# Kernel optimization log

Hardware: AMD Instinct MI355X
Metric: run time of the kernel (lower is better)

## Reference

```python
import jax, jax.numpy as jnp
import numpy as np
from jax import lax

B, T, N, H, M, L = 64, 12, 1000, 64, 4, 2


def _xavier(key, shape):
    fan_in, fan_out = shape[-2], shape[-1]
    scale = 1.414 * np.sqrt(2.0 / (fan_in + fan_out))
    return jax.random.normal(key, shape, dtype=jnp.float32) * scale


def setup_inputs() -> dict:
    key = jax.random.key(0)
    ks = jax.random.split(key, 20)
    inp = {
        "input": jax.random.normal(ks[0], (B, T, N, 1), dtype=jnp.float32),
        "init_hidden": jax.random.normal(ks[1], (L, B, N, H), dtype=jnp.float32),
        # scale dense diffusion supports ~row-stochastic magnitude to keep activations sane
        "supports": jax.random.normal(ks[2], (M, N, N), dtype=jnp.float32) * (1.0 / N),
        "teacher_force_ratio": 1,  # ratio 1.0 -> always teacher forcing (deterministic)
    }
    f0, f1 = 1 + H, H + H  # cat([input, state]) feature sizes for layer 0 / layer 1
    names = [("w0_r", "b0_r", f0), ("w0_u", "b0_u", f0), ("w0_c", "b0_c", f0),
             ("w1_r", "b1_r", f1), ("w1_u", "b1_u", f1), ("w1_c", "b1_c", f1)]
    for i, (wn, bn, f) in enumerate(names):
        inp[wn] = _xavier(ks[3 + i], (M, f, H))
        inp[bn] = jnp.zeros((H,), dtype=jnp.float32)
    inp["proj_w"] = _xavier(ks[10], (H, 1))
    inp["proj_b"] = jnp.zeros((1,), dtype=jnp.float32)
    return inp


def _gconv(supports, x, w, b):
    # supports [M,N,N], x [B,N,F], w [M,F,O] -> [B,N,O]
    aggr = jnp.einsum('jkm,iml->ijkl', supports, x)
    return jnp.einsum('ijkl,jlm->ikm', aggr, w) + b


def _cell(supports, x, h, wr, br, wu, bu, wc, bc):
    xs = jnp.concatenate([x, h], axis=2)
    r = jax.nn.sigmoid(_gconv(supports, xs, wr, br))
    u = jax.nn.sigmoid(_gconv(supports, xs, wu, bu))
    c = jnp.tanh(_gconv(supports, jnp.concatenate([x, r * h], axis=2), wc, bc))
    return u * h + (1.0 - u) * c


def reference(input, init_hidden, supports,
              w0_r, b0_r, w0_u, b0_u, w0_c, b0_c,
              w1_r, b1_r, w1_u, b1_u, w1_c, b1_c,
              proj_w, proj_b, teacher_force_ratio):
    # teacher_force_ratio == 1 -> current_input = input[:, t] at every step,
    # so step t (t=1..T-1) consumes input[:, t-1].
    def step(hidden, x_t):
        h0 = _cell(supports, x_t, hidden[0], w0_r, b0_r, w0_u, b0_u, w0_c, b0_c)
        h1 = _cell(supports, h0, hidden[1], w1_r, b1_r, w1_u, b1_u, w1_c, b1_c)
        out = h1 @ proj_w + proj_b  # [B,N,1]
        return jnp.stack([h0, h1], axis=0), out

    xs = jnp.transpose(input[:, :-1], (1, 0, 2, 3))  # [T-1,B,N,1]
    _, outs = lax.scan(step, init_hidden, xs)
    return jnp.transpose(outs, (1, 0, 2, 3))  # [B,T-1,N,1]
```

## Files before the change

kernel.cpp:

```cpp
#include <hip/hip_runtime.h>


#define BB 64
#define TT 12
#define NN 1000

typedef __bf16 bf16x8 __attribute__((ext_vector_type(8)));
typedef float f32x4 __attribute__((ext_vector_type(4)));
typedef unsigned short u16x8 __attribute__((ext_vector_type(8)));

__device__ __forceinline__ unsigned short f2b(float f) {
  union { float f; unsigned u; } x; x.f = f;
  unsigned u = x.u;
  u += 0x7FFFu + ((u >> 16) & 1u);
  return (unsigned short)(u >> 16);
}
__device__ __forceinline__ float b2f(unsigned short s) {
  union { float f; unsigned u; } x; x.u = ((unsigned)s) << 16; return x.f;
}

__device__ __forceinline__ void gload16(const void* g, void* l) {
  __builtin_amdgcn_global_load_lds((const __attribute__((address_space(1))) void*)g,
                                   (__attribute__((address_space(3))) void*)l, 16, 0, 0);
}


__global__ void prep_s_k(const float* __restrict__ S, unsigned short* __restrict__ Sb) {
  long idx = (long)blockIdx.x * 256 + threadIdx.x;
  if (idx >= 4194304L) return;
  int j = (int)(idx >> 20);
  int r = (int)((idx >> 10) & 1023);
  int c = (int)(idx & 1023);
  float v = (r < NN && c < NN) ? S[((long)j * NN + r) * NN + c] : 0.f;
  Sb[idx] = f2b(v);
}

__global__ void prep_wt_k(const float* __restrict__ wA, const float* __restrict__ wB,
                          unsigned short* __restrict__ WT, int F, int Fpad) {
  int Kt = 4 * Fpad;
  int idx = blockIdx.x * 256 + threadIdx.x;
  if (idx >= 128 * Kt) return;
  int o = idx / Kt, kk = idx % Kt;
  int j = kk / Fpad, l = kk % Fpad;
  float v = 0.f;
  if (l < F) {
    if (o < 64) v = wA ? wA[((long)j * F + l) * 64 + o] : 0.f;
    else        v = wB ? wB[((long)j * F + l) * 64 + (o - 64)] : 0.f;
  }
  WT[idx] = f2b(v);
}

__global__ void init_h2_k(const float* __restrict__ ih, float* __restrict__ H0,
                          float* __restrict__ H1) {
  long idx = (long)blockIdx.x * 256 + threadIdx.x;
  if (idx >= 4096000L) return;
  int b = (int)(idx / 64000);
  int rem = (int)(idx % 64000);
  int n = rem >> 6, o = rem & 63;
  long dst = ((long)((b << 10) | n)) * 64 + o;
  H0[dst] = ih[idx];
  H1[dst] = ih[4096000L + idx];
}

__global__ void build_xallT_k(const float* __restrict__ inp, unsigned short* __restrict__ XT) {
  unsigned idx = blockIdx.x * 256 + threadIdx.x;
  if (idx >= 786432u) return;
  int k = idx & 1023, row = idx >> 10;
  int t = row >> 6, b = row & 63;
  float v = (t < TT - 1 && k < NN) ? inp[((long)b * TT + t) * NN + k] : 0.f;
  XT[idx] = f2b(v);
}

__global__ void scatter_x_k(const unsigned short* __restrict__ XAG,
                            unsigned short* __restrict__ AG, int t) {
  unsigned idx = blockIdx.x * 256 + threadIdx.x;
  if (idx >= 262144u) return;
  int b = idx & 63, m = (idx >> 6) & 1023, j = idx >> 16;
  long base = ((long)((j << 10) | m)) * 6144 + b * 96;
  AG[base] = XAG[((long)((j << 10) | m)) * 768 + t * 64 + b];
  u16x8 z = {0, 0, 0, 0, 0, 0, 0, 0};
  *(u16x8*)(AG + base + 64) = z;
  *(u16x8*)(AG + base + 72) = z;
  *(u16x8*)(AG + base + 80) = z;
  *(u16x8*)(AG + base + 88) = z;
}

template <int RMUL>
__global__ void build_hT_k(const float* __restrict__ H, const unsigned short* __restrict__ RUb,
                           unsigned short* __restrict__ XT) {
  __shared__ float tile[128][65];
  int k0 = blockIdx.x * 128, b = blockIdx.y, tid = threadIdx.x;
  for (int q = 0; q < 32; ++q) {
    int kk = q * 4 + (tid >> 6), o = tid & 63;
    int k = k0 + kk;
    float v = 0.f;
    if (k < NN) {
      v = H[((long)((b << 10) | k)) * 64 + o];
      if (RMUL) v *= b2f(RUb[((long)(k * 64 + b)) * 128 + o]);
    }
    tile[kk][o] = v;
  }
  __syncthreads();
  for (int q = 0; q < 32; ++q) {
    int idx = q * 256 + tid;
    int o = idx >> 7, kk = idx & 127;
    XT[(((long)(b * 64 + o)) << 10) + k0 + kk] = f2b(tile[kk][o]);
  }
}

__global__ void build_h01T_k(const float* __restrict__ H0, const float* __restrict__ H1,
                             unsigned short* __restrict__ XT) {
  __shared__ float tile[128][65];
  int k0 = blockIdx.x * 128, b = blockIdx.y, tid = threadIdx.x;
  for (int src = 0; src < 2; ++src) {
    const float* H = src ? H1 : H0;
    if (src) __syncthreads();
    for (int q = 0; q < 32; ++q) {
      int kk = q * 4 + (tid >> 6), o = tid & 63;
      int k = k0 + kk;
      tile[kk][o] = (k < NN) ? H[((long)((b << 10) | k)) * 64 + o] : 0.f;
    }
    __syncthreads();
    for (int q = 0; q < 32; ++q) {
      int idx = q * 256 + tid;
      int o = idx >> 7, kk = idx & 127;
      XT[(((long)(b * 128 + src * 64 + o)) << 10) + k0 + kk] = f2b(tile[kk][o]);
    }
  }
}

template <int EPI>
__global__ __launch_bounds__(256)
void gemm_k(const unsigned short* __restrict__ A, long azstr, int lda, int acs, long ajstr,
            const unsigned short* __restrict__ BT, int ldb, int ksteps,
            void* __restrict__ Cv, long czstr, int ldc, int cstr, int coff,
            const float* __restrict__ p0, const void* __restrict__ p1v) {
  __shared__ unsigned short As[4096];
  __shared__ unsigned short Bs[4096];
  unsigned nwx = gridDim.x, nwy = gridDim.y;
  unsigned lid = blockIdx.x + nwx * (blockIdx.y + nwy * blockIdx.z);
  unsigned nwg = nwx * nwy * gridDim.z;
  unsigned swz = lid;
  if ((nwg & 7u) == 0) { unsigned cpx = nwg >> 3; swz = (lid & 7u) * cpx + (lid >> 3); }
  unsigned bx = swz % nwx;
  unsigned tmp = swz / nwx;
  unsigned by = tmp % nwy, bz = tmp / nwy;

  const int tid = threadIdx.x;
  const int lane = tid & 63;
  const int w = tid >> 6;
  const int wr = (w >> 1) * 64, wc = (w & 1) * 64;
  const long m0 = (long)bx * 128;
  const long n0 = (long)by * 128;
  A += (long)bz * azstr;

  const int rl = lane & 15;
  const int kb = (lane >> 4) * 8;
  const int s_r = tid >> 2;
  const int s_k = (tid & 3) * 8;

  f32x4 acc[4][4];
  for (int i = 0; i < 4; ++i)
    for (int j = 0; j < 4; ++j)
      acc[i][j] = (f32x4){0.f, 0.f, 0.f, 0.f};

  int jc = 0, lc = 0;
  for (int kt = 0; kt < ksteps; ++kt) {
    const unsigned short* Astep = A + (long)jc * ajstr + (long)lc * 32;
    const unsigned short* Bstep = BT + (long)kt * 32;
    gload16(Astep + (m0 + s_r) * (long)lda + s_k,       &As[tid * 8]);
    gload16(Astep + (m0 + 64 + s_r) * (long)lda + s_k,  &As[2048 + tid * 8]);
    gload16(Bstep + (n0 + s_r) * (long)ldb + s_k,       &Bs[tid * 8]);
    gload16(Bstep + (n0 + 64 + s_r) * (long)ldb + s_k,  &Bs[2048 + tid * 8]);
    __syncthreads();
    bf16x8 af[4], bg[4];
#pragma unroll
    for (int i = 0; i < 4; ++i) {
      af[i] = *(const bf16x8*)((const void*)&As[(wr + i * 16 + rl) * 32 + kb]);
      bg[i] = *(const bf16x8*)((const void*)&Bs[(wc + i * 16 + rl) * 32 + kb]);
    }
#pragma unroll
    for (int mi = 0; mi < 4; ++mi)
#pragma unroll
      for (int ni = 0; ni < 4; ++ni)
        acc[mi][ni] = __builtin_amdgcn_mfma_f32_16x16x32_bf16(af[mi], bg[ni], acc[mi][ni], 0, 0, 0);
    __syncthreads();
    if (++lc == acs) { lc = 0; ++jc; }
  }

  const int rb = (lane >> 4) * 4;
  const int cl = lane & 15;
  if constexpr (EPI == 3) {
    unsigned short* C = (unsigned short*)Cv + (long)bz * czstr;
#pragma unroll
    for (int mi = 0; mi < 4; ++mi) {
      long r = m0 + wr + mi * 16 + rb;
#pragma unroll
      for (int ni = 0; ni < 4; ++ni) {
        int c = (int)(n0 + wc + ni * 16 + cl);
        long cb = (long)(c >> 6) * cstr + coff + (c & 63);
#pragma unroll
        for (int jj = 0; jj < 4; ++jj)
          C[(r + jj) * (long)ldc + cb] = f2b(acc[mi][ni][jj]);
      }
    }
  } else if constexpr (EPI == 1) {
    unsigned short* RUo = (unsigned short*)Cv;
    const float* bu = (const float*)p1v;
#pragma unroll
    for (int mi = 0; mi < 4; ++mi) {
      long r = m0 + wr + mi * 16 + rb;
#pragma unroll
      for (int ni = 0; ni < 4; ++ni) {
        int c = (int)(n0 + wc + ni * 16 + cl);
        float bias = (c < 64) ? p0[c] : bu[c - 64];
#pragma unroll
        for (int jj = 0; jj < 4; ++jj) {
          float v = acc[mi][ni][jj] + bias;
          RUo[(r + jj) * 128 + c] = f2b(1.f / (1.f + __expf(-v)));
        }
      }
    }
  } else {
    float* H = (float*)Cv;
    const unsigned short* RUb = (const unsigned short*)p1v;
#pragma unroll
    for (int mi = 0; mi < 4; ++mi) {
      long r = m0 + wr + mi * 16 + rb;
#pragma unroll
      for (int ni = 0; ni < 4; ++ni) {
        int c = (int)(n0 + wc + ni * 16 + cl);
        if (c < 64) {
#pragma unroll
          for (int jj = 0; jj < 4; ++jj) {
            long rr = r + jj;
            float cv = tanhf(acc[mi][ni][jj] + p0[c]);
            float u = b2f(RUb[rr * 128 + 64 + c]);
            long ha = ((((rr & 63)) << 10) + (rr >> 6)) * 64 + c;
            H[ha] = u * H[ha] + (1.f - u) * cv;
          }
        }
      }
    }
  }
}

__global__ void proj_k(const float* __restrict__ H1, const float* __restrict__ pw,
                       const float* __restrict__ pb, float* __restrict__ out, int t) {
  __shared__ float tile[250][65];
  __shared__ float pws[64];
  int b = blockIdx.y, n0 = blockIdx.x * 250, tid = threadIdx.x;
  if (tid < 64) pws[tid] = pw[tid];
  for (int flat = tid; flat < 16000; flat += 256) {
    int nl = flat >> 6, o = flat & 63;
    tile[nl][o] = H1[((long)((b << 10) | (n0 + nl))) * 64 + o];
  }
  __syncthreads();
  if (tid < 250) {
    float s = pb[0];
#pragma unroll
    for (int o = 0; o < 64; ++o) s += tile[tid][o] * pws[o];
    out[((long)b * (TT - 1) + t) * NN + n0 + tid] = s;
  }
}

extern "C" void kernel_launch(void* const* d_in, const int* in_sizes, int n_in,
                              void* d_out, int out_size, void* d_ws, size_t ws_size,
                              hipStream_t stream) {
  const float* inp = (const float*)d_in[0];
  const float* ih  = (const float*)d_in[1];
  const float* sup = (const float*)d_in[2];
  const float* w0r = (const float*)d_in[4];
  const float* b0r = (const float*)d_in[5];
  const float* w0u = (const float*)d_in[6];
  const float* b0u = (const float*)d_in[7];
  const float* w0c = (const float*)d_in[8];
  const float* b0c = (const float*)d_in[9];
  const float* w1r = (const float*)d_in[10];
  const float* b1r = (const float*)d_in[11];
  const float* w1u = (const float*)d_in[12];
  const float* b1u = (const float*)d_in[13];
  const float* w1c = (const float*)d_in[14];
  const float* b1c = (const float*)d_in[15];
  const float* pw  = (const float*)d_in[16];
  const float* pb  = (const float*)d_in[17];
  float* out = (float*)d_out;

  char* ws = (char*)d_ws;
  unsigned short* Sb   = (unsigned short*)(ws + 0);
  unsigned short* AG   = (unsigned short*)(ws + 8388608);
  unsigned short* XT   = (unsigned short*)(ws + 75497472);
  unsigned short* XAG  = (unsigned short*)(ws + 92274688);
  unsigned short* RUb  = (unsigned short*)(ws + 98566144);
  float* H0            = (float*)(ws + 114950144);
  float* H1            = (float*)(ws + 131727360);
  unsigned short* Wru0 = (unsigned short*)(ws + 148504576);
  unsigned short* Wc0  = (unsigned short*)(ws + 148602880);
  unsigned short* Wru1 = (unsigned short*)(ws + 148701184);
  unsigned short* Wc1  = (unsigned short*)(ws + 148832256);

  prep_s_k<<<16384, 256, 0, stream>>>(sup, Sb);
  prep_wt_k<<<192, 256, 0, stream>>>(w0r, w0u, Wru0, 65, 96);
  prep_wt_k<<<192, 256, 0, stream>>>(w0c, nullptr, Wc0, 65, 96);
  prep_wt_k<<<256, 256, 0, stream>>>(w1r, w1u, Wru1, 128, 128);
  prep_wt_k<<<256, 256, 0, stream>>>(w1c, nullptr, Wc1, 128, 128);
  init_h2_k<<<16000, 256, 0, stream>>>(ih, H0, H1);
  build_xallT_k<<<3072, 256, 0, stream>>>(inp, XT);
  gemm_k<3><<<dim3(8, 6, 4), 256, 0, stream>>>(
      Sb, 1048576L, 1024, 32, 0, XT, 1024, 32, XAG, 786432L, 768, 64, 0, nullptr, nullptr);

  for (int t = 0; t < TT - 1; ++t) {
    scatter_x_k<<<1024, 256, 0, stream>>>(XAG, AG, t);
    build_hT_k<0><<<dim3(8, 64), 256, 0, stream>>>(H0, nullptr, XT);
    gemm_k<3><<<dim3(8, 32, 4), 256, 0, stream>>>(
        Sb, 1048576L, 1024, 32, 0, XT, 1024, 32, AG, 6291456L, 6144, 96, 1, nullptr, nullptr);
    gemm_k<1><<<dim3(500, 1, 1), 256, 0, stream>>>(
        AG, 0, 96, 3, 6291456L, Wru0, 384, 12, RUb, 0, 0, 0, 0, b0r, b0u);
    build_hT_k<1><<<dim3(8, 64), 256, 0, stream>>>(H0, RUb, XT);
    gemm_k<3><<<dim3(8, 32, 4), 256, 0, stream>>>(
        Sb, 1048576L, 1024, 32, 0, XT, 1024, 32, AG, 6291456L, 6144, 96, 1, nullptr, nullptr);
    gemm_k<4><<<dim3(500, 1, 1), 256, 0, stream>>>(
        AG, 0, 96, 3, 6291456L, Wc0, 384, 12, H0, 0, 0, 0, 0, b0c, RUb);
    build_h01T_k<<<dim3(8, 64), 256, 0, stream>>>(H0, H1, XT);
    gemm_k<3><<<dim3(8, 64, 4), 256, 0, stream>>>(
        Sb, 1048576L, 1024, 32, 0, XT, 1024, 32, AG, 8388608L, 8192, 64, 0, nullptr, nullptr);
    gemm_k<1><<<dim3(500, 1, 1), 256, 0, stream>>>(
        AG, 0, 128, 4, 8388608L, Wru1, 512, 16, RUb, 0, 0, 0, 0, b1r, b1u);
    build_hT_k<1><<<dim3(8, 64), 256, 0, stream>>>(H1, RUb, XT);
    gemm_k<3><<<dim3(8, 32, 4), 256, 0, stream>>>(
        Sb, 1048576L, 1024, 32, 0, XT, 1024, 32, AG, 8388608L, 8192, 128, 64, nullptr, nullptr);
    gemm_k<4><<<dim3(500, 1, 1), 256, 0, stream>>>(
        AG, 0, 128, 4, 8388608L, Wc1, 512, 16, H1, 0, 0, 0, 0, b1c, RUb);
    proj_k<<<dim3(4, 64), 256, 0, stream>>>(H1, pw, pb, out, t);
  }
}
```

Measured before the change: 5.210 ms.

## Add 256x256 double-buffered swizzled-LDS GEMM kernel for graph diffusion products

Adds a new 512-thread GEMM kernel with 256x256 output tiles, double-buffered LDS staging through direct global-to-LDS loads, XOR-swizzled LDS layout, and a schedule that interleaves barriers, MFMA and prefetch. It replaces the old 128x128 kernel for all support-by-state diffusion GEMMs. The goal is more data reuse per tile and overlap of memory loads with compute on these large K=1024 GEMMs. The cost is 128KB of LDS per block, fewer blocks per grid (wave quantisation) and hand-placed vmcnt waits that must match the staging order exactly. The block-index swizzle is also removed from the remaining small GEMM kernel.

Result: faster. 4.527 ms (-13.1%).

```diff
diff --git a/kernel.cpp b/kernel.cpp
--- a/kernel.cpp
+++ b/kernel.cpp
@@ -23,6 +23,10 @@
   __builtin_amdgcn_global_load_lds((const __attribute__((address_space(1))) void*)g,
                                    (__attribute__((address_space(3))) void*)l, 16, 0, 0);
 }
+
+#define FENCE asm volatile("" ::: "memory")
+#define BAR { FENCE; __builtin_amdgcn_s_barrier(); FENCE; }
+#define VMCNT(n) asm volatile("s_waitcnt vmcnt(" #n ")" ::: "memory")
 
 
 __global__ void prep_s_k(const float* __restrict__ S, unsigned short* __restrict__ Sb) {
@@ -129,6 +133,157 @@
   }
 }
 
+
+__device__ __forceinline__ void stageA256(const char* Ag, char* L, int s, int tid) {
+  int w = tid >> 6, l = tid & 63;
+#pragma unroll
+  for (int q = 0; q < 2; ++q) {
+    int row = s * 128 + (q * 8 + w) * 8 + (l >> 3);
+    int cb = ((l & 7) * 16) ^ ((row & 7) << 4);
+    gload16(Ag + (long)row * 2048 + cb, L + row * 128 + (l & 7) * 16);
+  }
+}
+__device__ __forceinline__ void stageB256(const char* Bg, char* L, int st, int tid) {
+  int w = tid >> 6, l = tid & 63;
+#pragma unroll
+  for (int q = 0; q < 2; ++q) {
+    int rr = (q * 8 + w) * 8 + (l >> 3);
+    int row = ((rr >> 5) << 6) + st * 32 + (rr & 31);
+    int cb = ((l & 7) * 16) ^ ((row & 7) << 4);
+    gload16(Bg + (long)row * 2048 + cb, L + row * 128 + (l & 7) * 16);
+  }
+}
+
+__device__ __forceinline__ void rdA(const char* L, bf16x8 (&af)[4][2], int rowbase, int l) {
+  int lr = l & 15, g = (l >> 4) * 16;
+#pragma unroll
+  for (int mi = 0; mi < 4; ++mi) {
+    int row = rowbase + mi * 16 + lr;
+#pragma unroll
+    for (int ks = 0; ks < 2; ++ks)
+      af[mi][ks] = *(const bf16x8*)(L + row * 128 + ((ks * 64 + g) ^ ((row & 7) << 4)));
+  }
+}
+template <int NI0>
+__device__ __forceinline__ void rdB(const char* L, bf16x8 (&bf)[4][2], int rowbase, int l) {
+  int lr = l & 15, g = (l >> 4) * 16;
+#pragma unroll
+  for (int ni = 0; ni < 2; ++ni) {
+    int row = rowbase + (NI0 + ni) * 16 + lr;
+#pragma unroll
+    for (int ks = 0; ks < 2; ++ks)
+      bf[NI0 + ni][ks] = *(const bf16x8*)(L + row * 128 + ((ks * 64 + g) ^ ((row & 7) << 4)));
+  }
+}
+template <int QM, int QN>
+__device__ __forceinline__ void mfmaQ(f32x4 (&acc)[8][4], bf16x8 (&af)[4][2],
+                                      bf16x8 (&bf)[4][2]) {
+  __builtin_amdgcn_s_setprio(1);
+#pragma unroll
+  for (int mi = 0; mi < 4; ++mi)
+#pragma unroll
+    for (int ni = 0; ni < 2; ++ni)
+#pragma unroll
+      for (int ks = 0; ks < 2; ++ks)
+        acc[QM * 4 + mi][QN * 2 + ni] = __builtin_amdgcn_mfma_f32_16x16x32_bf16(
+            af[mi][ks], bf[QN * 2 + ni][ks], acc[QM * 4 + mi][QN * 2 + ni], 0, 0, 0);
+  __builtin_amdgcn_s_setprio(0);
+}
+
+__global__ __launch_bounds__(512, 2)
+void gemm256_k(const unsigned short* __restrict__ A, long azstr,
+               const unsigned short* __restrict__ BT,
+               void* __restrict__ Cv, long czstr, int ldc, int cstr, int coff) {
+  alignas(16) __shared__ char lds[131072];
+  char* A0 = lds;
+  char* B0 = lds + 32768;
+  char* A1 = lds + 65536;
+  char* B1 = lds + 98304;
+
+  unsigned nwx = gridDim.x, nwy = gridDim.y;
+  unsigned lid = blockIdx.x + nwx * (blockIdx.y + nwy * blockIdx.z);
+  unsigned cpx = (nwx * nwy * gridDim.z) >> 3;
+  unsigned swz = (lid & 7u) * cpx + (lid >> 3);
+  unsigned bx = swz % nwx;
+  unsigned tmp = swz / nwx;
+  unsigned by = tmp % nwy, bz = tmp / nwy;
+
+  const int tid = threadIdx.x;
+  const int l = tid & 63;
+  const int w = tid >> 6;
+  const int wrb = (w >> 2) * 128;
+  const int wcb = (w & 3) * 64;
+  const long m0 = (long)bx * 256;
+  const long n0 = (long)by * 256;
+
+  const char* Ag = (const char*)A + (long)bz * azstr * 2 + m0 * 2048;
+  const char* Bg = (const char*)BT + n0 * 2048;
+
+  f32x4 acc[8][4];
+#pragma unroll
+  for (int i = 0; i < 8; ++i)
+#pragma unroll
+    for (int j = 0; j < 4; ++j)
+      acc[i][j] = (f32x4){0.f, 0.f, 0.f, 0.f};
+  bf16x8 af[4][2], bf[4][2];
+
+  stageB256(Bg, B0, 0, tid);
+  stageB256(Bg, B0, 1, tid);
+  stageA256(Ag, A0, 0, tid);
+  stageA256(Ag, A0, 1, tid);
+  stageB256(Bg + 128, B1, 0, tid);
+  stageB256(Bg + 128, B1, 1, tid);
+  stageA256(Ag + 128, A1, 0, tid);
+  VMCNT(6);
+  BAR;
+
+  for (int it = 0; it < 8; ++it) {
+    const bool L7 = (it == 7);
+    const int k0b = it * 256;
+    VMCNT(6);
+    rdA(A0, af, wrb, l);
+    rdB<0>(B0, bf, wcb, l);
+    stageA256(Ag + k0b + 128, A1, 1, tid);
+    BAR; mfmaQ<0, 0>(acc, af, bf); BAR;
+    rdB<2>(B0, bf, wcb, l);
+    if (!L7) stageB256(Bg + k0b + 256, B0, 0, tid);
+    BAR; mfmaQ<0, 1>(acc, af, bf); BAR;
+    rdA(A0, af, wrb + 64, l);
+    if (!L7) stageB256(Bg + k0b + 256, B0, 1, tid);
+    BAR; mfmaQ<1, 0>(acc, af, bf); BAR;
+    if (!L7) stageA256(Ag + k0b + 256, A0, 0, tid);
+    BAR; mfmaQ<1, 1>(acc, af, bf); BAR;
+    if (L7) { VMCNT(0); } else { VMCNT(6); }
+    rdA(A1, af, wrb, l);
+    rdB<0>(B1, bf, wcb, l);
+    if (!L7) stageA256(Ag + k0b + 256, A0, 1, tid);
+    BAR; mfmaQ<0, 0>(acc, af, bf); BAR;
+    rdB<2>(B1, bf, wcb, l);
+    if (!L7) stageB256(Bg + k0b + 384, B1, 0, tid);
+    BAR; mfmaQ<0, 1>(acc, af, bf); BAR;
+    rdA(A1, af, wrb + 64, l);
+    if (!L7) stageB256(Bg + k0b + 384, B1, 1, tid);
+    BAR; mfmaQ<1, 0>(acc, af, bf); BAR;
+    if (!L7) stageA256(Ag + k0b + 384, A1, 0, tid);
+    BAR; mfmaQ<1, 1>(acc, af, bf); BAR;
+  }
+
+  unsigned short* C = (unsigned short*)Cv + (long)bz * czstr;
+  const int rb = (l >> 4) * 4, cl = l & 15;
+#pragma unroll
+  for (int mi = 0; mi < 8; ++mi) {
+    long r = m0 + wrb + mi * 16 + rb;
+#pragma unroll
+    for (int ni = 0; ni < 4; ++ni) {
+      int c = (int)(n0 + wcb + ni * 16 + cl);
+      long cb = (long)(c >> 6) * cstr + coff + (c & 63);
+#pragma unroll
+      for (int jj = 0; jj < 4; ++jj)
+        C[(r + jj) * (long)ldc + cb] = f2b(acc[mi][ni][jj]);
+    }
+  }
+}
+
 template <int EPI>
 __global__ __launch_bounds__(256)
 void gemm_k(const unsigned short* __restrict__ A, long azstr, int lda, int acs, long ajstr,
@@ -137,14 +292,7 @@
             const float* __restrict__ p0, const void* __restrict__ p1v) {
   __shared__ unsigned short As[4096];
   __shared__ unsigned short Bs[4096];
-  unsigned nwx = gridDim.x, nwy = gridDim.y;
-  unsigned lid = blockIdx.x + nwx * (blockIdx.y + nwy * blockIdx.z);
-  unsigned nwg = nwx * nwy * gridDim.z;
-  unsigned swz = lid;
-  if ((nwg & 7u) == 0) { unsigned cpx = nwg >> 3; swz = (lid & 7u) * cpx + (lid >> 3); }
-  unsigned bx = swz % nwx;
-  unsigned tmp = swz / nwx;
-  unsigned by = tmp % nwy, bz = tmp / nwy;
+  unsigned bx = blockIdx.x, by = blockIdx.y, bz = blockIdx.z;
 
   const int tid = threadIdx.x;
   const int lane = tid & 63;
@@ -190,21 +338,7 @@
 
   const int rb = (lane >> 4) * 4;
   const int cl = lane & 15;
-  if constexpr (EPI == 3) {
-    unsigned short* C = (unsigned short*)Cv + (long)bz * czstr;
-#pragma unroll
-    for (int mi = 0; mi < 4; ++mi) {
-      long r = m0 + wr + mi * 16 + rb;
-#pragma unroll
-      for (int ni = 0; ni < 4; ++ni) {
-        int c = (int)(n0 + wc + ni * 16 + cl);
-        long cb = (long)(c >> 6) * cstr + coff + (c & 63);
-#pragma unroll
-        for (int jj = 0; jj < 4; ++jj)
-          C[(r + jj) * (long)ldc + cb] = f2b(acc[mi][ni][jj]);
-      }
-    }
-  } else if constexpr (EPI == 1) {
+  if constexpr (EPI == 1) {
     unsigned short* RUo = (unsigned short*)Cv;
     const float* bu = (const float*)p1v;
 #pragma unroll
@@ -306,29 +440,24 @@
   prep_wt_k<<<256, 256, 0, stream>>>(w1c, nullptr, Wc1, 128, 128);
   init_h2_k<<<16000, 256, 0, stream>>>(ih, H0, H1);
   build_xallT_k<<<3072, 256, 0, stream>>>(inp, XT);
-  gemm_k<3><<<dim3(8, 6, 4), 256, 0, stream>>>(
-      Sb, 1048576L, 1024, 32, 0, XT, 1024, 32, XAG, 786432L, 768, 64, 0, nullptr, nullptr);
+  gemm256_k<<<dim3(4, 3, 4), 512, 0, stream>>>(Sb, 1048576L, XT, XAG, 786432L, 768, 64, 0);
 
   for (int t = 0; t < TT - 1; ++t) {
     scatter_x_k<<<1024, 256, 0, stream>>>(XAG, AG, t);
     build_hT_k<0><<<dim3(8, 64), 256, 0, stream>>>(H0, nullptr, XT);
-    gemm_k<3><<<dim3(8, 32, 4), 256, 0, stream>>>(
-        Sb, 1048576L, 1024, 32, 0, XT, 1024, 32, AG, 6291456L, 6144, 96, 1, nullptr, nullptr);
+    gemm256_k<<<dim3(4, 16, 4), 512, 0, stream>>>(Sb, 1048576L, XT, AG, 6291456L, 6144, 96, 1);
     gemm_k<1><<<dim3(500, 1, 1), 256, 0, stream>>>(
         AG, 0, 96, 3, 6291456L, Wru0, 384, 12, RUb, 0, 0, 0, 0, b0r, b0u);
     build_hT_k<1><<<dim3(8, 64), 256, 0, stream>>>(H0, RUb, XT);
-    gemm_k<3><<<dim3(8, 32, 4), 256, 0, stream>>>(
-        Sb, 1048576L, 1024, 32, 0, XT, 1024, 32, AG, 6291456L, 6144, 96, 1, nullptr, nullptr);
+    gemm256_k<<<dim3(4, 16, 4), 512, 0, stream>>>(Sb, 1048576L, XT, AG, 6291456L, 6144, 96, 1);
     gemm_k<4><<<dim3(500, 1, 1), 256, 0, stream>>>(
         AG, 0, 96, 3, 6291456L, Wc0, 384, 12, H0, 0, 0, 0, 0, b0c, RUb);
     build_h01T_k<<<dim3(8, 64), 256, 0, stream>>>(H0, H1, XT);
-    gemm_k<3><<<dim3(8, 64, 4), 256, 0, stream>>>(
-        Sb, 1048576L, 1024, 32, 0, XT, 1024, 32, AG, 8388608L, 8192, 64, 0, nullptr, nullptr);
+    gemm256_k<<<dim3(4, 32, 4), 512, 0, stream>>>(Sb, 1048576L, XT, AG, 8388608L, 8192, 64, 0);
     gemm_k<1><<<dim3(500, 1, 1), 256, 0, stream>>>(
         AG, 0, 128, 4, 8388608L, Wru1, 512, 16, RUb, 0, 0, 0, 0, b1r, b1u);
     build_hT_k<1><<<dim3(8, 64), 256, 0, stream>>>(H1, RUb, XT);
-    gemm_k<3><<<dim3(8, 32, 4), 256, 0, stream>>>(
-        Sb, 1048576L, 1024, 32, 0, XT, 1024, 32, AG, 8388608L, 8192, 128, 64, nullptr, nullptr);
+    gemm256_k<<<dim3(4, 16, 4), 512, 0, stream>>>(Sb, 1048576L, XT, AG, 8388608L, 8192, 128, 64);
     gemm_k<4><<<dim3(500, 1, 1), 256, 0, stream>>>(
         AG, 0, 128, 4, 8388608L, Wc1, 512, 16, H1, 0, 0, 0, 0, b1c, RUb);
     proj_k<<<dim3(4, 64), 256, 0, stream>>>(H1, pw, pb, out, t);
```
